# Kernel tuning notes

Measured on AMD Instinct MI355X. Metric: run time of the kernel, lower is better.

Reference implementation:

```python
import jax, jax.numpy as jnp
import numpy as np

CHANNELS = 512
GROUPS = 32
EPS = 1e-6


def setup_inputs() -> dict:
    key = jax.random.key(0)
    ks = jax.random.split(key, 10)
    C = CHANNELS
    s = 1.0 / np.sqrt(C)
    return {
        "hidden_states": jax.random.normal(ks[0], (4, 64, 64, C), dtype=jnp.float32),
        "gn_scale": jnp.ones((C,), dtype=jnp.float32),
        "gn_bias": jnp.zeros((C,), dtype=jnp.float32),
        "wq": jax.random.normal(ks[1], (C, C), dtype=jnp.float32) * s,
        "bq": jnp.zeros((C,), dtype=jnp.float32),
        "wk": jax.random.normal(ks[2], (C, C), dtype=jnp.float32) * s,
        "bk": jnp.zeros((C,), dtype=jnp.float32),
        "wv": jax.random.normal(ks[3], (C, C), dtype=jnp.float32) * s,
        "bv": jnp.zeros((C,), dtype=jnp.float32),
        "wo": jax.random.normal(ks[4], (C, C), dtype=jnp.float32) * s,
        "bo": jnp.zeros((C,), dtype=jnp.float32),
    }


def reference(hidden_states, gn_scale, gn_bias, wq, bq, wk, bk, wv, bv, wo, bo):
    B, H, W, C = hidden_states.shape
    residual = hidden_states
    L = H * W
    x = hidden_states.reshape(B, L, C)

    # GroupNorm: stats over (spatial, channels-within-group), per batch per group
    xg = x.reshape(B, L, GROUPS, C // GROUPS)
    mean = jnp.mean(xg, axis=(1, 3), keepdims=True)
    var = jnp.var(xg, axis=(1, 3), keepdims=True)
    xn = ((xg - mean) * jax.lax.rsqrt(var + EPS)).reshape(B, L, C)
    xn = xn * gn_scale + gn_bias

    # QKV projections (heads=1, head_dim=C)
    q = xn @ wq + bq
    k = xn @ wk + bk
    v = xn @ wv + bv

    scale = 1.0 / jnp.sqrt(jnp.asarray(C, dtype=q.dtype))
    scores = jnp.einsum('bld,bsd->bls', q, k) * scale  # [B, L, L]
    attn = jax.nn.softmax(scores, axis=-1)
    out = jnp.einsum('bls,bsd->bld', attn, v)

    out = out @ wo + bo
    return out.reshape(B, H, W, C) + residual
```

## Files before the change

kernel.cpp:

```cpp
#include <hip/hip_runtime.h>
#include <hip/hip_bf16.h>
#include <stdint.h>

#define BATCH 4
#define SEQ   4096
#define CH    512
#define NGRP  32
#define GEPS  1e-6f

typedef short  short8  __attribute__((ext_vector_type(8)));
typedef float  floatx4 __attribute__((ext_vector_type(4)));

static __device__ __forceinline__ short bf16b(float f) {
    __hip_bfloat16 h = __float2bfloat16(f);
    return __builtin_bit_cast(short, h);
}
static __device__ __forceinline__ float bf2f(short s) {
    unsigned u = ((unsigned)(unsigned short)s) << 16;
    return __builtin_bit_cast(float, u);
}
static __device__ __forceinline__ char fp8b(float f) {
    int pk = __builtin_amdgcn_cvt_pk_fp8_f32(f, f, 0, false);
    return (char)(pk & 0xff);
}

static __device__ __forceinline__ void dma16(const void* g, void* l) {
    __builtin_amdgcn_global_load_lds(
        (const __attribute__((address_space(1))) unsigned int*)g,
        (__attribute__((address_space(3))) unsigned int*)l, 16, 0, 0);
}

static __device__ __forceinline__ float rowmax16(float x) {
    int xi = __builtin_bit_cast(int, x);
    x = fmaxf(x, __builtin_bit_cast(float, __builtin_amdgcn_update_dpp(xi, xi, 0x128, 0xf, 0xf, true)));
    xi = __builtin_bit_cast(int, x);
    x = fmaxf(x, __builtin_bit_cast(float, __builtin_amdgcn_update_dpp(xi, xi, 0x124, 0xf, 0xf, true)));
    xi = __builtin_bit_cast(int, x);
    x = fmaxf(x, __builtin_bit_cast(float, __builtin_amdgcn_update_dpp(xi, xi, 0x122, 0xf, 0xf, true)));
    xi = __builtin_bit_cast(int, x);
    x = fmaxf(x, __builtin_bit_cast(float, __builtin_amdgcn_update_dpp(xi, xi, 0x121, 0xf, 0xf, true)));
    return x;
}

__global__ __launch_bounds__(256) void gn_partial_kernel(const float* __restrict__ x,
                                                         float* __restrict__ statsraw) {
    int blk = blockIdx.x;
    int t = threadIdx.x;
    size_t row0 = (size_t)blk * 64;
    int qd = t & 127;
    int rh = t >> 7;
    const float* base = x + row0 * 512 + qd * 4;
    float s1 = 0.f, s2 = 0.f;
    #pragma unroll 4
    for (int i = 0; i < 32; ++i) {
        int r = rh + i * 2;
        float4 v = *reinterpret_cast<const float4*>(base + (size_t)r * 512);
        s1 += v.x + v.y + v.z + v.w;
        s2 += v.x * v.x + v.y * v.y + v.z * v.z + v.w * v.w;
    }
    __shared__ float a1[256], a2[256];
    a1[t] = s1; a2[t] = s2;
    __syncthreads();
    if (t < 32) {
        float u1 = 0.f, u2 = 0.f;
        #pragma unroll
        for (int e = 0; e < 4; ++e) {
            u1 += a1[t * 4 + e] + a1[128 + t * 4 + e];
            u2 += a2[t * 4 + e] + a2[128 + t * 4 + e];
        }
        int b = (int)(row0 >> 12);
        atomicAdd(&statsraw[(b * 32 + t) * 2],     u1);
        atomicAdd(&statsraw[(b * 32 + t) * 2 + 1], u2);
    }
}

__global__ __launch_bounds__(256) void gn_apply_kernel(const float* __restrict__ x,
                                                       const float* __restrict__ statsraw,
                                                       const float* __restrict__ gsc,
                                                       const float* __restrict__ gbs,
                                                       short* __restrict__ xn) {
    int i4 = blockIdx.x * 256 + threadIdx.x;
    int base = i4 * 4;
    int b = base >> 21;
    int c = base & 511;
    int sidx = (b * 32 + (c >> 4)) * 2;
    float s1 = statsraw[sidx], s2 = statsraw[sidx + 1];
    float mean = s1 * (1.f / 65536.f);
    float var  = s2 * (1.f / 65536.f) - mean * mean;
    float rstd = rsqrtf(var + GEPS);
    float4 xv = reinterpret_cast<const float4*>(x)[i4];
    float4 sv = *reinterpret_cast<const float4*>(gsc + c);
    float4 bv = *reinterpret_cast<const float4*>(gbs + c);
    union { short s[4]; uint2 u; } p;
    p.s[0] = bf16b((xv.x - mean) * rstd * sv.x + bv.x);
    p.s[1] = bf16b((xv.y - mean) * rstd * sv.y + bv.y);
    p.s[2] = bf16b((xv.z - mean) * rstd * sv.z + bv.z);
    p.s[3] = bf16b((xv.w - mean) * rstd * sv.w + bv.w);
    reinterpret_cast<uint2*>(xn)[i4] = p.u;
}

__global__ __launch_bounds__(256) void wtrans_kernel(const float* __restrict__ w0,
                                                     const float* __restrict__ w1,
                                                     const float* __restrict__ w2,
                                                     const float* __restrict__ w3,
                                                     short* __restrict__ wT) {
    const float* w = (blockIdx.z == 0) ? w0 : (blockIdx.z == 1) ? w1
                   : (blockIdx.z == 2) ? w2 : w3;
    short* out = wT + (size_t)blockIdx.z * CH * CH;
    int n0 = blockIdx.x * 32, k0 = blockIdx.y * 32;
    int tx = threadIdx.x, ty = threadIdx.y;
    __shared__ float s[32][33];
    #pragma unroll
    for (int i = 0; i < 4; ++i) {
        int kk = ty + i * 8;
        s[kk][tx] = w[(size_t)(k0 + kk) * CH + n0 + tx];
    }
    __syncthreads();
    #pragma unroll
    for (int i = 0; i < 4; ++i) {
        int nn = ty + i * 8;
        out[(size_t)(n0 + nn) * CH + k0 + tx] = bf16b(s[tx][nn]);
    }
}

__global__ __launch_bounds__(256) void gemm_qkv_kernel(const short* __restrict__ A,
                                                       const short* __restrict__ wT,
                                                       const float* __restrict__ bq,
                                                       const float* __restrict__ bk,
                                                       const float* __restrict__ bv,
                                                       char* __restrict__ q8,
                                                       char* __restrict__ k8,
                                                       char* __restrict__ vT8) {
    __shared__ short As[128 * 64];
    __shared__ short Bs[128 * 64];
    __shared__ char  vls[128 * 144];
    int m0 = blockIdx.x * 128;
    int nblk = blockIdx.y;
    int which = nblk >> 2;
    int n0 = (nblk & 3) * 128;
    const short* BT = wT + (size_t)which * 512 * 512;
    const float* bias = (which == 0) ? bq : (which == 1) ? bk : bv;
    int t = threadIdx.x;
    int w = t >> 6, lane = t & 63;
    int wr = w >> 1, wc = w & 1;
    int l15 = lane & 15, l4 = lane >> 4;
    floatx4 acc[4][4];
    #pragma unroll
    for (int i = 0; i < 4; ++i)
        #pragma unroll
        for (int j = 0; j < 4; ++j) acc[i][j] = (floatx4){0.f, 0.f, 0.f, 0.f};

    for (int k0 = 0; k0 < 512; k0 += 64) {
        __syncthreads();
        #pragma unroll
        for (int i = 0; i < 4; ++i) {
            int c = i * 256 + t;
            int row = c >> 3, j = (c & 7) ^ (row & 7);
            dma16(&A[(size_t)(m0 + row) * 512 + k0 + j * 8], &As[(c & ~63) * 8]);
            dma16(&BT[(size_t)(n0 + row) * 512 + k0 + j * 8], &Bs[(c & ~63) * 8]);
        }
        __syncthreads();
        #pragma unroll
        for (int kk = 0; kk < 64; kk += 32) {
            short8 af[4], bf[4];
            #pragma unroll
            for (int i = 0; i < 4; ++i) {
                int row = wr * 64 + i * 16 + l15;
                int j = (kk >> 3) + l4;
                af[i] = *reinterpret_cast<const short8*>(&As[(row * 8 + (j ^ (l15 & 7))) * 8]);
            }
            #pragma unroll
            for (int j2 = 0; j2 < 4; ++j2) {
                int row = wc * 64 + j2 * 16 + l15;
                int j = (kk >> 3) + l4;
                bf[j2] = *reinterpret_cast<const short8*>(&Bs[(row * 8 + (j ^ (l15 & 7))) * 8]);
            }
            #pragma unroll
            for (int i = 0; i < 4; ++i)
                #pragma unroll
                for (int j2 = 0; j2 < 4; ++j2)
                    acc[i][j2] = __builtin_amdgcn_mfma_f32_16x16x32_bf16(af[i], bf[j2], acc[i][j2], 0, 0, 0);
        }
    }
    if (which < 2) {
        char* o8 = (which == 0) ? q8 : k8;
        #pragma unroll
        for (int i = 0; i < 4; ++i)
            #pragma unroll
            for (int j = 0; j < 4; ++j)
                #pragma unroll
                for (int r = 0; r < 4; ++r) {
                    int row = m0 + wr * 64 + i * 16 + l4 * 4 + r;
                    int col = n0 + wc * 64 + j * 16 + l15;
                    o8[(size_t)row * 512 + col] = fp8b(acc[i][j][r] + bias[col]);
                }
    } else {
        __syncthreads();
        #pragma unroll
        for (int i = 0; i < 4; ++i)
            #pragma unroll
            for (int j = 0; j < 4; ++j)
                #pragma unroll
                for (int r = 0; r < 4; ++r) {
                    int rl = wr * 64 + i * 16 + l4 * 4 + r;
                    int rp = (rl & ~31) | (((rl & 15) << 1) | ((rl >> 4) & 1));
                    int cl = wc * 64 + j * 16 + l15;
                    vls[cl * 144 + rp] = fp8b(acc[i][j][r] + bias[n0 + cl]);
                }
        __syncthreads();
        int b = m0 >> 12, l0 = m0 & 4095;
        #pragma unroll
        for (int p = 0; p < 4; ++p) {
            int slot = p * 256 + t;
            int c = slot >> 3, off = (slot & 7) * 16;
            uint4 v;
            __builtin_memcpy(&v, &vls[c * 144 + off], 16);
            *reinterpret_cast<uint4*>(&vT8[((size_t)b * 512 + n0 + c) * 4096 + l0 + off]) = v;
        }
    }
}

__global__ __launch_bounds__(256) void gemm_bt_kernel(const short* __restrict__ Opart,
                                                      const float* __restrict__ ml,
                                                      const short* __restrict__ BT,
                                                      const float* __restrict__ bias,
                                                      float* __restrict__ outf,
                                                      const float* __restrict__ resid) {
    __shared__ short As[128 * 64];
    __shared__ short Bs[128 * 64];
    int m0 = blockIdx.x * 128, n0 = blockIdx.y * 128;
    int t = threadIdx.x;
    int w = t >> 6, lane = t & 63;
    int wr = w >> 1, wc = w & 1;
    int l15 = lane & 15, l4 = lane >> 4;
    const size_t PART = (size_t)BATCH * SEQ;
    floatx4 acc[4][4];
    #pragma unroll
    for (int i = 0; i < 4; ++i)
        #pragma unroll
        for (int j = 0; j < 4; ++j) acc[i][j] = (floatx4){0.f, 0.f, 0.f, 0.f};

    for (int k0 = 0; k0 < 512; k0 += 64) {
        __syncthreads();
        #pragma unroll
        for (int i = 0; i < 4; ++i) {
            int c = i * 256 + t;
            int rl = c >> 3, j = (c & 7) ^ (rl & 7);
            size_t rowg = (size_t)(m0 + rl);
            const short* s0 = Opart + rowg * 512 + k0 + j * 8;
            const short* s1 = s0 + PART * 512;
            uint4 a0 = *reinterpret_cast<const uint4*>(s0);
            uint4 a1 = *reinterpret_cast<const uint4*>(s1);
            float mA = ml[rowg * 2],          lA = ml[rowg * 2 + 1];
            float mB = ml[(PART + rowg) * 2], lB = ml[(PART + rowg) * 2 + 1];
            float mm = fmaxf(mA, mB);
            float e0 = __expf(mA - mm), e1 = __expf(mB - mm);
            float inv = 1.f / (e0 * lA + e1 * lB);
            e0 *= inv; e1 *= inv;
            union { uint4 u; short s[8]; } ua, ub, uo;
            ua.u = a0; ub.u = a1;
            #pragma unroll
            for (int e = 0; e < 8; ++e)
                uo.s[e] = bf16b(bf2f(ua.s[e]) * e0 + bf2f(ub.s[e]) * e1);
            *reinterpret_cast<uint4*>(&As[c * 8]) = uo.u;
            dma16(&BT[(size_t)(n0 + rl) * 512 + k0 + j * 8], &Bs[(c & ~63) * 8]);
        }
        __syncthreads();
        #pragma unroll
        for (int kk = 0; kk < 64; kk += 32) {
            short8 af[4], bf[4];
            #pragma unroll
            for (int i = 0; i < 4; ++i) {
                int row = wr * 64 + i * 16 + l15;
                int j = (kk >> 3) + l4;
                af[i] = *reinterpret_cast<const short8*>(&As[(row * 8 + (j ^ (l15 & 7))) * 8]);
            }
            #pragma unroll
            for (int j2 = 0; j2 < 4; ++j2) {
                int row = wc * 64 + j2 * 16 + l15;
                int j = (kk >> 3) + l4;
                bf[j2] = *reinterpret_cast<const short8*>(&Bs[(row * 8 + (j ^ (l15 & 7))) * 8]);
            }
            #pragma unroll
            for (int i = 0; i < 4; ++i)
                #pragma unroll
                for (int j2 = 0; j2 < 4; ++j2)
                    acc[i][j2] = __builtin_amdgcn_mfma_f32_16x16x32_bf16(af[i], bf[j2], acc[i][j2], 0, 0, 0);
        }
    }
    #pragma unroll
    for (int i = 0; i < 4; ++i)
        #pragma unroll
        for (int j = 0; j < 4; ++j)
            #pragma unroll
            for (int r = 0; r < 4; ++r) {
                int row = m0 + wr * 64 + i * 16 + l4 * 4 + r;
                int col = n0 + wc * 64 + j * 16 + l15;
                float vv = acc[i][j][r] + bias[col];
                outf[(size_t)row * 512 + col] = vv + resid[(size_t)row * 512 + col];
            }
}

__global__ __launch_bounds__(256, 2) void flash_kernel(const char* __restrict__ q8,
                                                       const char* __restrict__ k8,
                                                       const char* __restrict__ v8,
                                                       short* __restrict__ Opart,
                                                       float* __restrict__ ml) {
    __shared__ __align__(16) char smem[68096];
    int bx = blockIdx.x;
    int pb = bx & 7;
    int part = pb >> 2, b = pb & 3;
    int q0 = (bx >> 3) * 64;
    int t = threadIdx.x, w = t >> 6, lane = t & 63;
    int l15 = lane & 15, l4 = lane >> 4;
    const float scale = 0.044194173824159216f;

    long qf[16];
    {
        const char* qrow = q8 + ((size_t)b * SEQ + q0 + w * 16 + l15) * 512;
        #pragma unroll
        for (int ks = 0; ks < 16; ++ks)
            qf[ks] = *reinterpret_cast<const long*>(qrow + ks * 32 + l4 * 8);
    }

    floatx4 acc[32];
    #pragma unroll
    for (int i = 0; i < 32; ++i) acc[i] = (floatx4){0.f, 0.f, 0.f, 0.f};
    floatx4 lacc = (floatx4){0.f, 0.f, 0.f, 0.f};
    float mused[4] = {-1e30f, -1e30f, -1e30f, -1e30f};

    const long ones = 0x3838383838383838L;

    const char* kbase = k8 + (size_t)b * SEQ * 512;
    const char* vbase = v8 + (size_t)b * 512 * SEQ;

    const int kswz = l15 & 7;
    const int vswz = (l4 >> 1) ^ ((l15 >> 2) & 1);
    const int koff = (l4 & 1) * 8;
    const int s_begin = part * (SEQ / 2);

    auto stage = [&](int s0, int buf) {
        char* Kd = smem + buf * 16384;
        char* Vd = smem + 32768 + buf * 16384;
        #pragma unroll
        for (int i = 0; i < 4; ++i) {
            int c = i * 256 + t;
            int row = c >> 5, j = (c & 31) ^ (row & 7);
            dma16(kbase + (size_t)(s0 + row) * 512 + j * 16, Kd + (size_t)(c & ~63) * 16);
        }
        #pragma unroll
        for (int i = 0; i < 4; ++i) {
            int c = i * 256 + t;
            int d = c >> 1, j = (c & 1) ^ ((d >> 2) & 1);
            dma16(vbase + (size_t)d * SEQ + s0 + j * 16, Vd + (size_t)(c & ~63) * 16);
        }
    };

    stage(s_begin, 0);
    __syncthreads();

    for (int it = 0; it < 64; ++it) {
        int cur = it & 1;
        if (it + 1 < 64) stage(s_begin + (it + 1) * 32, 1 - cur);

        const char* Kb = smem + cur * 16384;
        const char* Vb = smem + 32768 + cur * 16384;

        floatx4 sa0 = (floatx4){0.f, 0.f, 0.f, 0.f};
        floatx4 sa1 = (floatx4){0.f, 0.f, 0.f, 0.f};
        #pragma unroll
        for (int ks = 0; ks < 16; ++ks) {
            int jc = ks * 2 + (l4 >> 1);
            int a0 = (l15 * 32 + (jc ^ kswz)) * 16 + koff;
            long b0 = *reinterpret_cast<const long*>(Kb + a0);
            long b1 = *reinterpret_cast<const long*>(Kb + a0 + 8192);
            sa0 = __builtin_amdgcn_mfma_f32_16x16x32_fp8_fp8(qf[ks], b0, sa0, 0, 0, 0);
            sa1 = __builtin_amdgcn_mfma_f32_16x16x32_fp8_fp8(qf[ks], b1, sa1, 0, 0, 0);
        }

        float v0[4], v1[4], nm4[4];
        bool need = false;
        #pragma unroll
        for (int r = 0; r < 4; ++r) {
            v0[r] = sa0[r] * scale; v1[r] = sa1[r] * scale;
            nm4[r] = rowmax16(fmaxf(v0[r], v1[r]));
            need |= (nm4[r] > mused[r] + 5.0f);
        }
        if (__ballot(need)) {
            #pragma unroll
            for (int r = 0; r < 4; ++r) {
                float nm = fmaxf(mused[r], nm4[r]);
                float al = __expf(mused[r] - nm);
                lacc[r] *= al;
                #pragma unroll
                for (int i = 0; i < 32; ++i) acc[i][r] *= al;
                mused[r] = nm;
            }
        }
        float p0[4], p1[4];
        #pragma unroll
        for (int r = 0; r < 4; ++r) {
            p0[r] = __expf(v0[r] - mused[r]);
            p1[r] = __expf(v1[r] - mused[r]);
        }

        char* Ps = smem + 65536 + w * 640;
        #pragma unroll
        for (int r = 0; r < 4; ++r) {
            int pk = __builtin_amdgcn_cvt_pk_fp8_f32(p0[r], p1[r], 0, false);
            *reinterpret_cast<short*>(Ps + (l4 * 4 + r) * 40 + l15 * 2) = (short)pk;
        }

        long pf;
        __builtin_memcpy(&pf, (const char*)__builtin_assume_aligned(Ps + l15 * 40 + l4 * 8, 8), 8);
        lacc = __builtin_amdgcn_mfma_f32_16x16x32_fp8_fp8(pf, ones, lacc, 0, 0, 0);
        #pragma unroll
        for (int tt = 0; tt < 32; ++tt) {
            int d = tt * 16 + l15;
            long vf = *reinterpret_cast<const long*>(Vb + (d * 2 + vswz) * 16 + koff);
            acc[tt] = __builtin_amdgcn_mfma_f32_16x16x32_fp8_fp8(pf, vf, acc[tt], 0, 0, 0);
        }

        __syncthreads();
    }

    short* obase = Opart + (((size_t)part * BATCH + b) * SEQ + q0 + w * 16) * 512;
    #pragma unroll
    for (int r = 0; r < 4; ++r) {
        #pragma unroll
        for (int tt = 0; tt < 32; ++tt)
            obase[(size_t)(l4 * 4 + r) * 512 + tt * 16 + l15] = bf16b(acc[tt][r]);
    }
    if (l15 == 0) {
        #pragma unroll
        for (int r = 0; r < 4; ++r) {
            size_t rowg = ((size_t)part * BATCH + b) * SEQ + q0 + w * 16 + l4 * 4 + r;
            ml[rowg * 2]     = mused[r];
            ml[rowg * 2 + 1] = lacc[r];
        }
    }
}

extern "C" void kernel_launch(void* const* d_in, const int* in_sizes, int n_in,
                              void* d_out, int out_size, void* d_ws, size_t ws_size,
                              hipStream_t stream) {
    const float* x   = (const float*)d_in[0];
    const float* gsc = (const float*)d_in[1];
    const float* gbs = (const float*)d_in[2];
    const float* wq  = (const float*)d_in[3];
    const float* bq  = (const float*)d_in[4];
    const float* wk  = (const float*)d_in[5];
    const float* bk  = (const float*)d_in[6];
    const float* wv  = (const float*)d_in[7];
    const float* bv  = (const float*)d_in[8];
    const float* wo  = (const float*)d_in[9];
    const float* bo  = (const float*)d_in[10];
    float* out = (float*)d_out;

    char* ws = (char*)d_ws;
    const size_t MB = 1ull << 20;
    short* xn    = (short*)ws;
    char*  q8    = (char*)(ws + 16 * MB);
    char*  k8    = (char*)(ws + 24 * MB);
    char*  vT8   = (char*)(ws + 32 * MB);
    short* Opart = (short*)(ws + 40 * MB);
    short* wT    = (short*)(ws + 72 * MB);
    float* stats = (float*)(ws + 74 * MB);
    float* ml    = (float*)(ws + 74 * MB + 65536);

    hipMemsetAsync(stats, 0, 256 * sizeof(float), stream);
    gn_partial_kernel<<<256, 256, 0, stream>>>(x, stats);
    gn_apply_kernel<<<8192, 256, 0, stream>>>(x, stats, gsc, gbs, xn);
    wtrans_kernel<<<dim3(16, 16, 4), dim3(32, 8), 0, stream>>>(wq, wk, wv, wo, wT);

    short* woT = wT + 786432;

    gemm_qkv_kernel<<<dim3(128, 12), 256, 0, stream>>>(xn, wT, bq, bk, bv, q8, k8, vT8);
    flash_kernel<<<512, 256, 0, stream>>>(q8, k8, vT8, Opart, ml);
    gemm_bt_kernel<<<dim3(128, 4), 256, 0, stream>>>(Opart, ml, woT, bo, out, x);
}
```

Measured before the change: 321.7 us.

## Split flash attention head dimension across wave pairs with warp-specialized softmax and loads

```diff
diff --git a/kernel.cpp b/kernel.cpp
--- a/kernel.cpp
+++ b/kernel.cpp
@@ -301,31 +301,32 @@
             }
 }
 
-__global__ __launch_bounds__(256, 2) void flash_kernel(const char* __restrict__ q8,
+__global__ __launch_bounds__(512, 4) void flash_kernel(const char* __restrict__ q8,
                                                        const char* __restrict__ k8,
                                                        const char* __restrict__ v8,
                                                        short* __restrict__ Opart,
                                                        float* __restrict__ ml) {
-    __shared__ __align__(16) char smem[68096];
+    __shared__ __align__(16) char smem[76608];
     int bx = blockIdx.x;
     int pb = bx & 7;
     int part = pb >> 2, b = pb & 3;
     int q0 = (bx >> 3) * 64;
     int t = threadIdx.x, w = t >> 6, lane = t & 63;
+    int qg = w >> 1, dg = w & 1;
     int l15 = lane & 15, l4 = lane >> 4;
     const float scale = 0.044194173824159216f;
 
-    long qf[16];
+    long qf[8];
     {
-        const char* qrow = q8 + ((size_t)b * SEQ + q0 + w * 16 + l15) * 512;
-        #pragma unroll
-        for (int ks = 0; ks < 16; ++ks)
+        const char* qrow = q8 + ((size_t)b * SEQ + q0 + qg * 16 + l15) * 512 + dg * 256;
+        #pragma unroll
+        for (int ks = 0; ks < 8; ++ks)
             qf[ks] = *reinterpret_cast<const long*>(qrow + ks * 32 + l4 * 8);
     }
 
-    floatx4 acc[32];
-    #pragma unroll
-    for (int i = 0; i < 32; ++i) acc[i] = (floatx4){0.f, 0.f, 0.f, 0.f};
+    floatx4 acc[16];
+    #pragma unroll
+    for (int i = 0; i < 16; ++i) acc[i] = (floatx4){0.f, 0.f, 0.f, 0.f};
     floatx4 lacc = (floatx4){0.f, 0.f, 0.f, 0.f};
     float mused[4] = {-1e30f, -1e30f, -1e30f, -1e30f};
 
@@ -333,108 +334,156 @@
 
     const char* kbase = k8 + (size_t)b * SEQ * 512;
     const char* vbase = v8 + (size_t)b * 512 * SEQ;
+    const int s_begin = part * (SEQ / 2);
+
+    char* Sq  = smem + 65536 + qg * 2048;
+    char* Ps  = smem + 73728 + qg * 640;
+    char* alr = smem + 76288 + qg * 80;
 
     const int kswz = l15 & 7;
     const int vswz = (l4 >> 1) ^ ((l15 >> 2) & 1);
     const int koff = (l4 & 1) * 8;
-    const int s_begin = part * (SEQ / 2);
-
-    auto stage = [&](int s0, int buf) {
-        char* Kd = smem + buf * 16384;
-        char* Vd = smem + 32768 + buf * 16384;
-        #pragma unroll
-        for (int i = 0; i < 4; ++i) {
-            int c = i * 256 + t;
+
+    {
+        char* Kd = smem;
+        char* Vd = smem + 32768;
+        #pragma unroll
+        for (int i = 0; i < 2; ++i) {
+            int c = i * 512 + t;
             int row = c >> 5, j = (c & 31) ^ (row & 7);
-            dma16(kbase + (size_t)(s0 + row) * 512 + j * 16, Kd + (size_t)(c & ~63) * 16);
-        }
-        #pragma unroll
-        for (int i = 0; i < 4; ++i) {
-            int c = i * 256 + t;
+            dma16(kbase + (size_t)(s_begin + row) * 512 + j * 16, Kd + (size_t)(c & ~63) * 16);
+        }
+        #pragma unroll
+        for (int i = 0; i < 2; ++i) {
+            int c = i * 512 + t;
             int d = c >> 1, j = (c & 1) ^ ((d >> 2) & 1);
-            dma16(vbase + (size_t)d * SEQ + s0 + j * 16, Vd + (size_t)(c & ~63) * 16);
-        }
-    };
-
-    stage(s_begin, 0);
+            dma16(vbase + (size_t)d * SEQ + s_begin + j * 16, Vd + (size_t)(c & ~63) * 16);
+        }
+    }
+    asm volatile("s_waitcnt vmcnt(0)" ::: "memory");
     __syncthreads();
 
     for (int it = 0; it < 64; ++it) {
         int cur = it & 1;
-        if (it + 1 < 64) stage(s_begin + (it + 1) * 32, 1 - cur);
-
         const char* Kb = smem + cur * 16384;
         const char* Vb = smem + 32768 + cur * 16384;
 
         floatx4 sa0 = (floatx4){0.f, 0.f, 0.f, 0.f};
         floatx4 sa1 = (floatx4){0.f, 0.f, 0.f, 0.f};
-        #pragma unroll
-        for (int ks = 0; ks < 16; ++ks) {
-            int jc = ks * 2 + (l4 >> 1);
+        __builtin_amdgcn_s_setprio(1);
+        #pragma unroll
+        for (int ks = 0; ks < 8; ++ks) {
+            int jc = dg * 16 + ks * 2 + (l4 >> 1);
             int a0 = (l15 * 32 + (jc ^ kswz)) * 16 + koff;
             long b0 = *reinterpret_cast<const long*>(Kb + a0);
             long b1 = *reinterpret_cast<const long*>(Kb + a0 + 8192);
             sa0 = __builtin_amdgcn_mfma_f32_16x16x32_fp8_fp8(qf[ks], b0, sa0, 0, 0, 0);
             sa1 = __builtin_amdgcn_mfma_f32_16x16x32_fp8_fp8(qf[ks], b1, sa1, 0, 0, 0);
         }
-
-        float v0[4], v1[4], nm4[4];
-        bool need = false;
-        #pragma unroll
-        for (int r = 0; r < 4; ++r) {
-            v0[r] = sa0[r] * scale; v1[r] = sa1[r] * scale;
-            nm4[r] = rowmax16(fmaxf(v0[r], v1[r]));
-            need |= (nm4[r] > mused[r] + 5.0f);
-        }
-        if (__ballot(need)) {
+        __builtin_amdgcn_s_setprio(0);
+        if (!dg) {
+            *reinterpret_cast<floatx4*>(Sq + lane * 16)        = sa0;
+            *reinterpret_cast<floatx4*>(Sq + 1024 + lane * 16) = sa1;
+        }
+        __syncthreads();
+
+        if (dg) {
+            floatx4 o0 = *reinterpret_cast<const floatx4*>(Sq + lane * 16);
+            floatx4 o1 = *reinterpret_cast<const floatx4*>(Sq + 1024 + lane * 16);
+            float v0[4], v1[4], nm4[4];
+            bool need = false;
             #pragma unroll
             for (int r = 0; r < 4; ++r) {
-                float nm = fmaxf(mused[r], nm4[r]);
-                float al = __expf(mused[r] - nm);
-                lacc[r] *= al;
-                #pragma unroll
-                for (int i = 0; i < 32; ++i) acc[i][r] *= al;
-                mused[r] = nm;
-            }
-        }
-        float p0[4], p1[4];
-        #pragma unroll
-        for (int r = 0; r < 4; ++r) {
-            p0[r] = __expf(v0[r] - mused[r]);
-            p1[r] = __expf(v1[r] - mused[r]);
-        }
-
-        char* Ps = smem + 65536 + w * 640;
-        #pragma unroll
-        for (int r = 0; r < 4; ++r) {
-            int pk = __builtin_amdgcn_cvt_pk_fp8_f32(p0[r], p1[r], 0, false);
-            *reinterpret_cast<short*>(Ps + (l4 * 4 + r) * 40 + l15 * 2) = (short)pk;
+                v0[r] = (sa0[r] + o0[r]) * scale;
+                v1[r] = (sa1[r] + o1[r]) * scale;
+                nm4[r] = rowmax16(fmaxf(v0[r], v1[r]));
+                need |= (nm4[r] > mused[r] + 5.0f);
+            }
+            int flg = (__ballot(need) != 0ull) ? 1 : 0;
+            if (flg) {
+                floatx4 alv;
+                #pragma unroll
+                for (int r = 0; r < 4; ++r) {
+                    float nm = fmaxf(mused[r], nm4[r]);
+                    float al = __expf(mused[r] - nm);
+                    lacc[r] *= al;
+                    #pragma unroll
+                    for (int i = 0; i < 16; ++i) acc[i][r] *= al;
+                    mused[r] = nm;
+                    alv[r] = al;
+                }
+                if (l15 == 0)
+                    *reinterpret_cast<floatx4*>(alr + l4 * 16) = alv;
+            }
+            if (lane == 0) *reinterpret_cast<int*>(alr + 64) = flg;
+            #pragma unroll
+            for (int r = 0; r < 4; ++r) {
+                v0[r] = __expf(v0[r] - mused[r]);
+                v1[r] = __expf(v1[r] - mused[r]);
+            }
+            #pragma unroll
+            for (int r = 0; r < 4; ++r) {
+                int pk = __builtin_amdgcn_cvt_pk_fp8_f32(v0[r], v1[r], 0, false);
+                *reinterpret_cast<short*>(Ps + (l4 * 4 + r) * 40 + l15 * 2) = (short)pk;
+            }
+        } else {
+            if (it + 1 < 64) {
+                int s0 = s_begin + (it + 1) * 32;
+                char* Kd = smem + (1 - cur) * 16384;
+                char* Vd = smem + 32768 + (1 - cur) * 16384;
+                int u = qg * 64 + lane;
+                #pragma unroll
+                for (int i = 0; i < 4; ++i) {
+                    int c = i * 256 + u;
+                    int row = c >> 5, j = (c & 31) ^ (row & 7);
+                    dma16(kbase + (size_t)(s0 + row) * 512 + j * 16, Kd + (size_t)(c & ~63) * 16);
+                }
+                #pragma unroll
+                for (int i = 0; i < 4; ++i) {
+                    int c = i * 256 + u;
+                    int d = c >> 1, j = (c & 1) ^ ((d >> 2) & 1);
+                    dma16(vbase + (size_t)d * SEQ + s0 + j * 16, Vd + (size_t)(c & ~63) * 16);
+                }
+            }
+            asm volatile("s_waitcnt vmcnt(0)" ::: "memory");
+        }
+        __syncthreads();
+
+        if (!dg) {
+            int flg = *reinterpret_cast<const int*>(alr + 64);
+            if (flg) {
+                floatx4 alv = *reinterpret_cast<const floatx4*>(alr + l4 * 16);
+                #pragma unroll
+                for (int i = 0; i < 16; ++i)
+                    #pragma unroll
+                    for (int r = 0; r < 4; ++r) acc[i][r] *= alv[r];
+            }
         }
 
         long pf;
         __builtin_memcpy(&pf, (const char*)__builtin_assume_aligned(Ps + l15 * 40 + l4 * 8, 8), 8);
-        lacc = __builtin_amdgcn_mfma_f32_16x16x32_fp8_fp8(pf, ones, lacc, 0, 0, 0);
-        #pragma unroll
-        for (int tt = 0; tt < 32; ++tt) {
-            int d = tt * 16 + l15;
+        if (dg) lacc = __builtin_amdgcn_mfma_f32_16x16x32_fp8_fp8(pf, ones, lacc, 0, 0, 0);
+        __builtin_amdgcn_s_setprio(1);
+        #pragma unroll
+        for (int tt = 0; tt < 16; ++tt) {
+            int d = dg * 256 + tt * 16 + l15;
             long vf = *reinterpret_cast<const long*>(Vb + (d * 2 + vswz) * 16 + koff);
             acc[tt] = __builtin_amdgcn_mfma_f32_16x16x32_fp8_fp8(pf, vf, acc[tt], 0, 0, 0);
         }
-
-        __syncthreads();
-    }
-
-    short* obase = Opart + (((size_t)part * BATCH + b) * SEQ + q0 + w * 16) * 512;
+        __builtin_amdgcn_s_setprio(0);
+    }
+
+    short* obase = Opart + (((size_t)part * BATCH + b) * SEQ + q0 + qg * 16) * 512 + dg * 256;
     #pragma unroll
     for (int r = 0; r < 4; ++r) {
         #pragma unroll
-        for (int tt = 0; tt < 32; ++tt)
+        for (int tt = 0; tt < 16; ++tt)
             obase[(size_t)(l4 * 4 + r) * 512 + tt * 16 + l15] = bf16b(acc[tt][r]);
     }
-    if (l15 == 0) {
+    if (dg && l15 == 0) {
         #pragma unroll
         for (int r = 0; r < 4; ++r) {
-            size_t rowg = ((size_t)part * BATCH + b) * SEQ + q0 + w * 16 + l4 * 4 + r;
+            size_t rowg = ((size_t)part * BATCH + b) * SEQ + q0 + qg * 16 + l4 * 4 + r;
             ml[rowg * 2]     = mused[r];
             ml[rowg * 2 + 1] = lacc[r];
         }
@@ -476,6 +525,6 @@
     short* woT = wT + 786432;
 
     gemm_qkv_kernel<<<dim3(128, 12), 256, 0, stream>>>(xn, wT, bq, bk, bv, q8, k8, vT8);
-    flash_kernel<<<512, 256, 0, stream>>>(q8, k8, vT8, Opart, ml);
+    flash_kernel<<<512, 512, 0, stream>>>(q8, k8, vT8, Opart, ml);
     gemm_bt_kernel<<<dim3(128, 4), 256, 0, stream>>>(Opart, ml, woT, bo, out, x);
 }
```

Measured after the change: 429.6 us. 33.5% more time.

## Pre-tile K and V fp8 into MFMA-friendly blocks for 16-byte LDS reads

Applied to the files above, without the earlier changes.

```diff
diff --git a/kernel.cpp b/kernel.cpp
--- a/kernel.cpp
+++ b/kernel.cpp
@@ -10,6 +10,7 @@
 
 typedef short  short8  __attribute__((ext_vector_type(8)));
 typedef float  floatx4 __attribute__((ext_vector_type(4)));
+typedef long   longx2  __attribute__((ext_vector_type(2)));
 
 static __device__ __forceinline__ short bf16b(float f) {
     __hip_bfloat16 h = __float2bfloat16(f);
@@ -182,8 +183,7 @@
                     acc[i][j2] = __builtin_amdgcn_mfma_f32_16x16x32_bf16(af[i], bf[j2], acc[i][j2], 0, 0, 0);
         }
     }
-    if (which < 2) {
-        char* o8 = (which == 0) ? q8 : k8;
+    if (which == 0) {
         #pragma unroll
         for (int i = 0; i < 4; ++i)
             #pragma unroll
@@ -192,7 +192,22 @@
                 for (int r = 0; r < 4; ++r) {
                     int row = m0 + wr * 64 + i * 16 + l4 * 4 + r;
                     int col = n0 + wc * 64 + j * 16 + l15;
-                    o8[(size_t)row * 512 + col] = fp8b(acc[i][j][r] + bias[col]);
+                    q8[(size_t)row * 512 + col] = fp8b(acc[i][j][r] + bias[col]);
+                }
+    } else if (which == 1) {
+        #pragma unroll
+        for (int i = 0; i < 4; ++i)
+            #pragma unroll
+            for (int j = 0; j < 4; ++j)
+                #pragma unroll
+                for (int r = 0; r < 4; ++r) {
+                    int row = m0 + wr * 64 + i * 16 + l4 * 4 + r;
+                    int col = n0 + wc * 64 + j * 16 + l15;
+                    int bb = row >> 12, s = row & 4095;
+                    size_t idx = (size_t)bb * 2097152 + (size_t)(s >> 5) * 16384
+                               + (s & 15) * 1024 + ((s >> 4) & 1) * 8
+                               + (col >> 3) * 16 + (col & 7);
+                    k8[idx] = fp8b(acc[i][j][r] + bias[col]);
                 }
     } else {
         __syncthreads();
@@ -215,7 +230,16 @@
             int c = slot >> 3, off = (slot & 7) * 16;
             uint4 v;
             __builtin_memcpy(&v, &vls[c * 144 + off], 16);
-            *reinterpret_cast<uint4*>(&vT8[((size_t)b * 512 + n0 + c) * 4096 + l0 + off]) = v;
+            int dcol = n0 + c;
+            int g = dcol >> 5, rr = dcol & 15, h = (dcol >> 4) & 1;
+            int s = l0 + off;
+            int sb = s >> 5, mb = (s & 31) >> 3;
+            char* dst = vT8 + (size_t)b * 2097152 + (size_t)sb * 16384
+                      + (size_t)((((g * 16 + rr) * 4 + mb) * 16) + h * 8);
+            unsigned long long lo = ((unsigned long long)v.y << 32) | v.x;
+            unsigned long long hi = ((unsigned long long)v.w << 32) | v.z;
+            *reinterpret_cast<unsigned long long*>(dst)      = lo;
+            *reinterpret_cast<unsigned long long*>(dst + 16) = hi;
         }
     }
 }
@@ -334,34 +358,35 @@
     const char* kbase = k8 + (size_t)b * SEQ * 512;
     const char* vbase = v8 + (size_t)b * 512 * SEQ;
 
-    const int kswz = l15 & 7;
-    const int vswz = (l4 >> 1) ^ ((l15 >> 2) & 1);
-    const int koff = (l4 & 1) * 8;
-    const int s_begin = part * (SEQ / 2);
-
-    auto stage = [&](int s0, int buf) {
+    const int ksw = l15 & 7;
+    const int vsw = (l15 >> 1) & 3;
+    const int sb0 = part * 64;
+
+    auto stage = [&](int sb, int buf) {
         char* Kd = smem + buf * 16384;
         char* Vd = smem + 32768 + buf * 16384;
+        const char* kt = kbase + (size_t)sb * 16384;
+        const char* vt = vbase + (size_t)sb * 16384;
         #pragma unroll
         for (int i = 0; i < 4; ++i) {
             int c = i * 256 + t;
-            int row = c >> 5, j = (c & 31) ^ (row & 7);
-            dma16(kbase + (size_t)(s0 + row) * 512 + j * 16, Kd + (size_t)(c & ~63) * 16);
+            int src = (c & ~63) | ((c & 63) ^ ((c >> 6) & 7));
+            dma16(kt + (size_t)src * 16, Kd + (size_t)(c & ~63) * 16);
         }
         #pragma unroll
         for (int i = 0; i < 4; ++i) {
             int c = i * 256 + t;
-            int d = c >> 1, j = (c & 1) ^ ((d >> 2) & 1);
-            dma16(vbase + (size_t)d * SEQ + s0 + j * 16, Vd + (size_t)(c & ~63) * 16);
+            int src = (c & ~3) | ((c & 3) ^ ((c >> 3) & 3));
+            dma16(vt + (size_t)src * 16, Vd + (size_t)(c & ~63) * 16);
         }
     };
 
-    stage(s_begin, 0);
+    stage(sb0, 0);
     __syncthreads();
 
     for (int it = 0; it < 64; ++it) {
         int cur = it & 1;
-        if (it + 1 < 64) stage(s_begin + (it + 1) * 32, 1 - cur);
+        if (it + 1 < 64) stage(sb0 + it + 1, 1 - cur);
 
         const char* Kb = smem + cur * 16384;
         const char* Vb = smem + 32768 + cur * 16384;
@@ -370,12 +395,10 @@
         floatx4 sa1 = (floatx4){0.f, 0.f, 0.f, 0.f};
         #pragma unroll
         for (int ks = 0; ks < 16; ++ks) {
-            int jc = ks * 2 + (l4 >> 1);
-            int a0 = (l15 * 32 + (jc ^ kswz)) * 16 + koff;
-            long b0 = *reinterpret_cast<const long*>(Kb + a0);
-            long b1 = *reinterpret_cast<const long*>(Kb + a0 + 8192);
-            sa0 = __builtin_amdgcn_mfma_f32_16x16x32_fp8_fp8(qf[ks], b0, sa0, 0, 0, 0);
-            sa1 = __builtin_amdgcn_mfma_f32_16x16x32_fp8_fp8(qf[ks], b1, sa1, 0, 0, 0);
+            longx2 kk = *reinterpret_cast<const longx2*>(
+                Kb + ((l15 * 64 + ((ks * 4 + l4) ^ ksw)) << 4));
+            sa0 = __builtin_amdgcn_mfma_f32_16x16x32_fp8_fp8(qf[ks], kk[0], sa0, 0, 0, 0);
+            sa1 = __builtin_amdgcn_mfma_f32_16x16x32_fp8_fp8(qf[ks], kk[1], sa1, 0, 0, 0);
         }
 
         float v0[4], v1[4], nm4[4];
@@ -415,10 +438,11 @@
         __builtin_memcpy(&pf, (const char*)__builtin_assume_aligned(Ps + l15 * 40 + l4 * 8, 8), 8);
         lacc = __builtin_amdgcn_mfma_f32_16x16x32_fp8_fp8(pf, ones, lacc, 0, 0, 0);
         #pragma unroll
-        for (int tt = 0; tt < 32; ++tt) {
-            int d = tt * 16 + l15;
-            long vf = *reinterpret_cast<const long*>(Vb + (d * 2 + vswz) * 16 + koff);
-            acc[tt] = __builtin_amdgcn_mfma_f32_16x16x32_fp8_fp8(pf, vf, acc[tt], 0, 0, 0);
+        for (int g = 0; g < 16; ++g) {
+            longx2 vv = *reinterpret_cast<const longx2*>(
+                Vb + ((((g * 16 + l15) * 4) + (l4 ^ vsw)) << 4));
+            acc[2 * g]     = __builtin_amdgcn_mfma_f32_16x16x32_fp8_fp8(pf, vv[0], acc[2 * g],     0, 0, 0);
+            acc[2 * g + 1] = __builtin_amdgcn_mfma_f32_16x16x32_fp8_fp8(pf, vv[1], acc[2 * g + 1], 0, 0, 0);
         }
 
         __syncthreads();
```

Measured after the change: 289.0 us. 10.2% less time.
